# Kernel tuning notes

Hardware: AMD Instinct MI355X
Metric: run time of the kernel (lower is better)

## Reference

```python
import jax, jax.numpy as jnp
import numpy as np

HID = 1024
HEADS = 16
HEAD_DIM = HID // HEADS
MAX_REL = 2


def _rel_embed(table, length_q, length_k):
    # table: [2*MAX_REL+1, head_dim] -> [len_q, len_k, head_dim]
    dist = jnp.arange(length_k)[None, :] - jnp.arange(length_q)[:, None]
    idx = jnp.clip(dist, -MAX_REL, MAX_REL) + MAX_REL
    return table[idx]


def setup_inputs() -> dict:
    key = jax.random.key(0)
    ks = jax.random.split(key, 16)
    B, S = 2, 2048
    bound = 1.0 / np.sqrt(HID)

    def lin(k1, k2):
        W = jax.random.uniform(k1, (HID, HID), jnp.float32, -bound, bound)
        b = jax.random.uniform(k2, (HID,), jnp.float32, -bound, bound)
        return W, b

    Wq, bq = lin(ks[0], ks[1])
    Wk, bk = lin(ks[2], ks[3])
    Wv, bv = lin(ks[4], ks[5])
    Wo, bo = lin(ks[6], ks[7])
    # xavier_uniform for [5, head_dim] tables
    xav = np.sqrt(6.0 / (2 * MAX_REL + 1 + HEAD_DIM))
    rel_k = jax.random.uniform(ks[8], (2 * MAX_REL + 1, HEAD_DIM), jnp.float32, -xav, xav)
    rel_v = jax.random.uniform(ks[9], (2 * MAX_REL + 1, HEAD_DIM), jnp.float32, -xav, xav)
    return {
        'key': jax.random.normal(ks[10], (B, S, HID), jnp.float32),
        'query': jax.random.normal(ks[11], (B, S, HID), jnp.float32),
        'value': jax.random.normal(ks[12], (B, S, HID), jnp.float32),
        'Wq': Wq, 'bq': bq, 'Wk': Wk, 'bk': bk, 'Wv': Wv, 'bv': bv,
        'Wo': Wo, 'bo': bo, 'rel_k': rel_k, 'rel_v': rel_v,
    }


def reference(key, query, value, Wq, bq, Wk, bk, Wv, bv, Wo, bo, rel_k, rel_v):
    B, Lq, _ = query.shape
    Lk = key.shape[1]
    q = query @ Wq.T + bq   # [B, Lq, HID]
    k = key @ Wk.T + bk     # [B, Lk, HID]
    v = value @ Wv.T + bv   # [B, Lk, HID]

    qh = q.reshape(B, Lq, HEADS, HEAD_DIM).transpose(0, 2, 1, 3)  # [B,H,Lq,D]
    kh = k.reshape(B, Lk, HEADS, HEAD_DIM).transpose(0, 2, 1, 3)
    vh = v.reshape(B, Lk, HEADS, HEAD_DIM).transpose(0, 2, 1, 3)

    attn1 = jnp.einsum('bhqd,bhkd->bhqk', qh, kh)
    rk = _rel_embed(rel_k, Lq, Lk)                                # [Lq,Lk,D]
    attn2 = jnp.einsum('bhqd,qkd->bhqk', qh, rk)
    scale = jnp.sqrt(jnp.float32(HEAD_DIM))
    attn = jax.nn.softmax((attn1 + attn2) / scale, axis=-1)      # [B,H,Lq,Lk]

    w1 = jnp.einsum('bhqk,bhkd->bhqd', attn, vh)
    rv = _rel_embed(rel_v, Lq, Lk)                                # [Lq,Lk,D]
    w2 = jnp.einsum('bhqk,qkd->bhqd', attn, rv)

    x = (w1 + w2).transpose(0, 2, 1, 3).reshape(B, Lq, HID)
    return x @ Wo.T + bo
```

## Files before the change

kernel.cpp:

```cpp
#include <hip/hip_runtime.h>
#include <hip/hip_bf16.h>

#define S_LEN 2048
#define HID_DIM 1024
#define NH 16
#define HD 64
#define MTOT 4096

typedef __attribute__((ext_vector_type(8))) short short8;
typedef __attribute__((ext_vector_type(4))) float f32x4;

__device__ __forceinline__ float bf2f(unsigned short u) {
  union { unsigned int i; float f; } x; x.i = ((unsigned int)u) << 16; return x.f;
}
__device__ __forceinline__ unsigned short f2bf(float f) {
  union { float ff; unsigned int i; } x; x.ff = f;
  return (unsigned short)((x.i + 0x7fffu + ((x.i >> 16) & 1u)) >> 16);
}
__device__ __forceinline__ unsigned short f2bf_rna(float f) {
  union { float ff; unsigned int i; } x; x.ff = f;
  return (unsigned short)((x.i + 0x8000u) >> 16);
}
__device__ __forceinline__ f32x4 mfma16(short8 a, short8 b, f32x4 c) {
  return __builtin_amdgcn_mfma_f32_16x16x32_bf16(a, b, c, 0, 0, 0);
}
__device__ __forceinline__ void gl_lds16(const unsigned short* g, unsigned short* l) {
  __builtin_amdgcn_global_load_lds(
      (const __attribute__((address_space(1))) unsigned int*)g,
      (__attribute__((address_space(3))) unsigned int*)l, 16, 0, 0);
}

__global__ __launch_bounds__(256) void cvt3(const float* __restrict__ a, const float* __restrict__ b,
                                            const float* __restrict__ c, unsigned short* __restrict__ oa,
                                            unsigned short* __restrict__ ob, unsigned short* __restrict__ oc,
                                            int n4) {
  int i = blockIdx.x * 256 + threadIdx.x;
  if (i >= n4) return;
  const float* src = blockIdx.y == 0 ? a : blockIdx.y == 1 ? b : c;
  unsigned short* dst = blockIdx.y == 0 ? oa : blockIdx.y == 1 ? ob : oc;
  float4 v = reinterpret_cast<const float4*>(src)[i];
  union { unsigned short u[4]; unsigned long long ll; } o;
  o.u[0] = f2bf(v.x); o.u[1] = f2bf(v.y); o.u[2] = f2bf(v.z); o.u[3] = f2bf(v.w);
  reinterpret_cast<unsigned long long*>(dst)[i] = o.ll;
}
__global__ __launch_bounds__(256) void cvt4(const float* __restrict__ a, const float* __restrict__ b,
                                            const float* __restrict__ c, const float* __restrict__ d,
                                            unsigned short* __restrict__ oa, unsigned short* __restrict__ ob,
                                            unsigned short* __restrict__ oc, unsigned short* __restrict__ od,
                                            int n4) {
  int i = blockIdx.x * 256 + threadIdx.x;
  if (i >= n4) return;
  const float* src = blockIdx.y == 0 ? a : blockIdx.y == 1 ? b : blockIdx.y == 2 ? c : d;
  unsigned short* dst = blockIdx.y == 0 ? oa : blockIdx.y == 1 ? ob : blockIdx.y == 2 ? oc : od;
  float4 v = reinterpret_cast<const float4*>(src)[i];
  union { unsigned short u[4]; unsigned long long ll; } o;
  o.u[0] = f2bf(v.x); o.u[1] = f2bf(v.y); o.u[2] = f2bf(v.z); o.u[3] = f2bf(v.w);
  reinterpret_cast<unsigned long long*>(dst)[i] = o.ll;
}

__device__ __forceinline__ void gemm_core(const unsigned short* __restrict__ A,
                                          const unsigned short* __restrict__ W,
                                          unsigned short* As, unsigned short* Bs,
                                          int m0, int n0, f32x4 (&acc)[4][4]) {
  const int tid = threadIdx.x;
  const int lane = tid & 63;
  const int wrow = (tid >> 6) >> 1, wcol = (tid >> 6) & 1;
  const int lr = lane & 15, g = lane >> 4;
  const int r = tid >> 2, c8 = (tid & 3) * 8;
  const unsigned short* ag0 = A + (size_t)(m0 + r) * HID_DIM + c8;
  const unsigned short* ag1 = ag0 + (size_t)64 * HID_DIM;
  const unsigned short* bg0 = W + (size_t)(n0 + r) * HID_DIM + c8;
  const unsigned short* bg1 = bg0 + (size_t)64 * HID_DIM;
  unsigned short* al0 = As + r * 32 + c8;
  unsigned short* al1 = al0 + 64 * 32;
  unsigned short* bl0 = Bs + r * 32 + c8;
  unsigned short* bl1 = bl0 + 64 * 32;
  for (int k0 = 0; k0 < HID_DIM; k0 += 32) {
    __syncthreads();
    gl_lds16(ag0 + k0, al0);
    gl_lds16(ag1 + k0, al1);
    gl_lds16(bg0 + k0, bl0);
    gl_lds16(bg1 + k0, bl1);
    __syncthreads();
    short8 af[4], bfr[4];
#pragma unroll
    for (int m = 0; m < 4; ++m)
      af[m] = *reinterpret_cast<const short8*>(&As[(wrow * 64 + m * 16 + lr) * 32 + g * 8]);
#pragma unroll
    for (int n = 0; n < 4; ++n)
      bfr[n] = *reinterpret_cast<const short8*>(&Bs[(wcol * 64 + n * 16 + lr) * 32 + g * 8]);
#pragma unroll
    for (int m = 0; m < 4; ++m)
#pragma unroll
      for (int n = 0; n < 4; ++n)
        acc[m][n] = mfma16(af[m], bfr[n], acc[m][n]);
  }
}

__global__ __launch_bounds__(256) void qkv_gemm(
    const unsigned short* __restrict__ Aq, const unsigned short* __restrict__ Ak,
    const unsigned short* __restrict__ Av,
    const unsigned short* __restrict__ Wq, const unsigned short* __restrict__ Wk,
    const unsigned short* __restrict__ Wv,
    const float* __restrict__ bq, const float* __restrict__ bk, const float* __restrict__ bv,
    unsigned short* __restrict__ Qp, unsigned short* __restrict__ Kp,
    unsigned short* __restrict__ Vt) {
  __shared__ __attribute__((aligned(16))) unsigned short As[128 * 32];
  __shared__ __attribute__((aligned(16))) unsigned short Bs[128 * 32];
  const int which = blockIdx.x >> 3;
  const int n0 = (blockIdx.x & 7) * 128;
  const int m0 = blockIdx.y * 128;
  const unsigned short* A = which == 0 ? Aq : which == 1 ? Ak : Av;
  const unsigned short* W = which == 0 ? Wq : which == 1 ? Wk : Wv;
  const float* bias = which == 0 ? bq : which == 1 ? bk : bv;

  f32x4 acc[4][4];
  const f32x4 vzero = {0.f, 0.f, 0.f, 0.f};
#pragma unroll
  for (int m = 0; m < 4; ++m)
#pragma unroll
    for (int n = 0; n < 4; ++n) acc[m][n] = vzero;

  gemm_core(A, W, As, Bs, m0, n0, acc);

  const int lane = threadIdx.x & 63;
  const int wrow = (threadIdx.x >> 6) >> 1, wcol = (threadIdx.x >> 6) & 1;
  const int lr = lane & 15, g = lane >> 4;
  const float scl = (which == 0) ? 0.125f : 1.0f;
#pragma unroll
  for (int m = 0; m < 4; ++m) {
    const int rbase = m0 + wrow * 64 + m * 16 + g * 4;
#pragma unroll
    for (int n = 0; n < 4; ++n) {
      const int col = n0 + wcol * 64 + n * 16 + lr;
      const float bcol = bias[col];
      if (which < 2) {
        unsigned short* O = which == 0 ? Qp : Kp;
#pragma unroll
        for (int rg = 0; rg < 4; ++rg)
          O[(size_t)(rbase + rg) * HID_DIM + col] = f2bf((acc[m][n][rg] + bcol) * scl);
      } else {
        const int bb = rbase >> 11, s = rbase & 2047;
        const int h = col >> 6, d = col & 63;
        union { unsigned short u[4]; unsigned long long ll; } o;
#pragma unroll
        for (int rg = 0; rg < 4; ++rg) o.u[rg] = f2bf(acc[m][n][rg] + bcol);
        *reinterpret_cast<unsigned long long*>(
            &Vt[((size_t)(bb * NH + h) * HD + d) * S_LEN + s]) = o.ll;
      }
    }
  }
}

__global__ __launch_bounds__(256) void out_gemm(const unsigned short* __restrict__ X,
                                                const unsigned short* __restrict__ Wo,
                                                const float* __restrict__ bo,
                                                float* __restrict__ out) {
  __shared__ __attribute__((aligned(16))) unsigned short As[128 * 32];
  __shared__ __attribute__((aligned(16))) unsigned short Bs[128 * 32];
  const int n0 = blockIdx.x * 128;
  const int m0 = blockIdx.y * 128;
  f32x4 acc[4][4];
  const f32x4 vzero = {0.f, 0.f, 0.f, 0.f};
#pragma unroll
  for (int m = 0; m < 4; ++m)
#pragma unroll
    for (int n = 0; n < 4; ++n) acc[m][n] = vzero;

  gemm_core(X, Wo, As, Bs, m0, n0, acc);

  const int lane = threadIdx.x & 63;
  const int wrow = (threadIdx.x >> 6) >> 1, wcol = (threadIdx.x >> 6) & 1;
  const int lr = lane & 15, g = lane >> 4;
#pragma unroll
  for (int m = 0; m < 4; ++m) {
    const int rbase = m0 + wrow * 64 + m * 16 + g * 4;
#pragma unroll
    for (int n = 0; n < 4; ++n) {
      const int col = n0 + wcol * 64 + n * 16 + lr;
      const float bcol = bo[col];
#pragma unroll
      for (int rg = 0; rg < 4; ++rg)
        out[(size_t)(rbase + rg) * HID_DIM + col] = acc[m][n][rg] + bcol;
    }
  }
}

__global__ __launch_bounds__(512, 2) void attn_kernel(
    const unsigned short* __restrict__ Qp, const unsigned short* __restrict__ Kp,
    const unsigned short* __restrict__ Vt, const float* __restrict__ relk,
    const float* __restrict__ relv, unsigned short* __restrict__ Xa) {
  __shared__ __attribute__((aligned(16))) unsigned short kv[2][8192];
  __shared__ __attribute__((aligned(16))) unsigned short Ps[8][16][72];
  __shared__ float projs[128][5];
  __shared__ float relks[5][64];
  __shared__ float rvs[5][64];

  const int tid = threadIdx.x;
  const int lane = tid & 63;
  const int w = tid >> 6;
  const int lr = lane & 15, g = lane >> 4;
  const int virt = (blockIdx.x & 7) * 64 + (blockIdx.x >> 3);
  const int bh = virt >> 4;
  const int qbase = (virt & 15) * 128;
  const int b = bh >> 4, h = bh & 15;

  const unsigned short* Qg = Qp + ((size_t)(b * S_LEN + qbase)) * HID_DIM + h * HD;
  const unsigned short* Kg = Kp + ((size_t)b * S_LEN) * HID_DIM + h * HD;
  const unsigned short* Vg = Vt + (size_t)bh * HD * S_LEN;

#pragma unroll
  for (int i = 0; i < 2; ++i) {
    const int flat = i * 8192 + tid * 16;
    const int row = flat >> 7, c = (flat >> 4) & 7;
    gl_lds16(Qg + (size_t)row * HID_DIM + ((c ^ (row & 7)) * 8), &kv[1][flat >> 1]);
  }
  {
    const int flat = tid * 16;
    const int row = flat >> 7, c = (flat >> 4) & 7;
    const int csrc = (c ^ (row & 7)) * 8;
    gl_lds16(Kg + (size_t)row * HID_DIM + csrc, &kv[0][flat >> 1]);
    gl_lds16(Vg + (size_t)row * S_LEN + csrc, &kv[0][4096 + (flat >> 1)]);
  }
  for (int i = tid; i < 320; i += 512) {
    ((float*)relks)[i] = relk[i];
    ((float*)rvs)[i] = relv[i];
  }
  __syncthreads();

  for (int idx = tid; idx < 640; idx += 512) {
    const int row = idx & 127, j = idx >> 7;
    float acc = 0.f;
    for (int d = 0; d < 64; ++d)
      acc += bf2f(kv[1][row * 64 + ((d >> 3) ^ (row & 7)) * 8 + (d & 7)]) * relks[j][d];
    projs[row][j] = acc;
  }
  short8 aq[2];
#pragma unroll
  for (int h2 = 0; h2 < 2; ++h2) {
    const int row = w * 16 + lr;
    aq[h2] = *reinterpret_cast<const short8*>(
        &kv[1][row * 64 + (((g + 4 * h2) ^ (lr & 7)) * 8)]);
  }
  __syncthreads();

  float pj0[4], pj4[4];
#pragma unroll
  for (int i = 0; i < 4; ++i) {
    const int qloc = w * 16 + g * 4 + i;
    pj0[i] = projs[qloc][0];
    pj4[i] = projs[qloc][4];
  }

  const f32x4 vzero = {0.f, 0.f, 0.f, 0.f};
  f32x4 accO[4];
#pragma unroll
  for (int n = 0; n < 4; ++n) accO[n] = vzero;
  float sp0[4], sp4[4], sv1[4], sv2[4], sv3[4];
#pragma unroll
  for (int i = 0; i < 4; ++i) {
    sp0[i] = 0.f; sp4[i] = 0.f; sv1[i] = 0.f; sv2[i] = 0.f; sv3[i] = 0.f;
  }
  const int Qw = qbase + w * 16;

  for (int t = 0; t < 32; ++t) {
    const int kb = t * 64;
    const unsigned short* Ks = kv[t & 1];
    const unsigned short* Vs = Ks + 4096;
    if (t < 31) {
      const int kb2 = kb + 64;
      unsigned short* dst = &kv[(t + 1) & 1][0];
      const int flat = tid * 16;
      const int row = flat >> 7, c = (flat >> 4) & 7;
      const int csrc = (c ^ (row & 7)) * 8;
      gl_lds16(Kg + (size_t)(kb2 + row) * HID_DIM + csrc, dst + (flat >> 1));
      gl_lds16(Vg + (size_t)row * S_LEN + kb2 + csrc, dst + 4096 + (flat >> 1));
    }
    short8 kf[4][2];
#pragma unroll
    for (int n = 0; n < 4; ++n)
#pragma unroll
      for (int h2 = 0; h2 < 2; ++h2)
        kf[n][h2] = *reinterpret_cast<const short8*>(
            &Ks[(n * 16 + lr) * 64 + (((g + 4 * h2) ^ (lr & 7)) * 8)]);
    f32x4 accS[4];
#pragma unroll
    for (int n = 0; n < 4; ++n) {
      f32x4 z = mfma16(aq[0], kf[n][0], vzero);
      accS[n] = mfma16(aq[1], kf[n][1], z);
    }

    const bool mixed = (kb + 63 >= Qw - 2) && (kb <= Qw + 17);
    if (!mixed) {
      const bool left = kb < Qw;
#pragma unroll
      for (int n = 0; n < 4; ++n)
#pragma unroll
        for (int r = 0; r < 4; ++r) {
          const float p = __expf(accS[n][r] + (left ? pj0[r] : pj4[r]));
          if (left) sp0[r] += p; else sp4[r] += p;
          Ps[w][g * 4 + r][n * 16 + lr] = f2bf_rna(p);
        }
    } else {
#pragma unroll
      for (int n = 0; n < 4; ++n) {
        const int kg = kb + n * 16 + lr;
#pragma unroll
        for (int r = 0; r < 4; ++r) {
          const int qloc = w * 16 + g * 4 + r;
          const int dist = kg - (qbase + qloc);
          float pjv;
          if (dist <= -2) pjv = pj0[r];
          else if (dist >= 2) pjv = pj4[r];
          else pjv = projs[qloc][dist + 2];
          const float p = __expf(accS[n][r] + pjv);
          if (dist <= -2) sp0[r] += p;
          else if (dist >= 2) sp4[r] += p;
          else if (dist == -1) sv1[r] += p;
          else if (dist == 0) sv2[r] += p;
          else sv3[r] += p;
          Ps[w][g * 4 + r][n * 16 + lr] = f2bf_rna(p);
        }
      }
    }
    asm volatile("" ::: "memory");
    short8 vf[4][2];
#pragma unroll
    for (int n = 0; n < 4; ++n)
#pragma unroll
      for (int h2 = 0; h2 < 2; ++h2)
        vf[n][h2] = *reinterpret_cast<const short8*>(
            &Vs[(n * 16 + lr) * 64 + (((g + 4 * h2) ^ (lr & 7)) * 8)]);
    short8 pa0 = *reinterpret_cast<const short8*>(&Ps[w][lr][g * 8]);
    short8 pa1 = *reinterpret_cast<const short8*>(&Ps[w][lr][g * 8 + 32]);
#pragma unroll
    for (int n = 0; n < 4; ++n) {
      accO[n] = mfma16(pa0, vf[n][0], accO[n]);
      accO[n] = mfma16(pa1, vf[n][1], accO[n]);
    }
    __syncthreads();
  }

#pragma unroll
  for (int i = 0; i < 4; ++i) {
    float v0 = sp0[i], v1 = sv1[i], v2 = sv2[i], v3 = sv3[i], v4 = sp4[i];
#pragma unroll
    for (int s = 1; s <= 8; s <<= 1) {
      v0 += __shfl_xor(v0, s); v1 += __shfl_xor(v1, s); v2 += __shfl_xor(v2, s);
      v3 += __shfl_xor(v3, s); v4 += __shfl_xor(v4, s);
    }
    const float rl = 1.f / (v0 + v1 + v2 + v3 + v4);
    const int qrow = b * S_LEN + qbase + w * 16 + g * 4 + i;
#pragma unroll
    for (int n = 0; n < 4; ++n) {
      const int d = n * 16 + lr;
      const float val = (accO[n][i] + v0 * rvs[0][d] + v1 * rvs[1][d] +
                         v2 * rvs[2][d] + v3 * rvs[3][d] + v4 * rvs[4][d]) * rl;
      Xa[(size_t)qrow * HID_DIM + h * HD + d] = f2bf(val);
    }
  }
}

extern "C" void kernel_launch(void* const* d_in, const int* in_sizes, int n_in,
                              void* d_out, int out_size, void* d_ws, size_t ws_size,
                              hipStream_t stream) {
  (void)in_sizes; (void)n_in; (void)out_size; (void)ws_size;
  const float* f_key   = (const float*)d_in[0];
  const float* f_query = (const float*)d_in[1];
  const float* f_value = (const float*)d_in[2];
  const float* Wq = (const float*)d_in[3];
  const float* bq = (const float*)d_in[4];
  const float* Wk = (const float*)d_in[5];
  const float* bk = (const float*)d_in[6];
  const float* Wv = (const float*)d_in[7];
  const float* bv = (const float*)d_in[8];
  const float* Wo = (const float*)d_in[9];
  const float* bo = (const float*)d_in[10];
  const float* relk = (const float*)d_in[11];
  const float* relv = (const float*)d_in[12];

  char* ws = (char*)d_ws;
  const size_t SZ = (size_t)MTOT * HID_DIM * sizeof(unsigned short);
  unsigned short* cq  = (unsigned short*)(ws + 0 * SZ);
  unsigned short* ck  = (unsigned short*)(ws + 1 * SZ);
  unsigned short* cv  = (unsigned short*)(ws + 2 * SZ);
  unsigned short* wqb = (unsigned short*)(ws + 3 * SZ);
  unsigned short* wkb = wqb + 1024 * 1024;
  unsigned short* wvb = wkb + 1024 * 1024;
  unsigned short* wob = wvb + 1024 * 1024;
  unsigned short* Qp  = (unsigned short*)(ws + 4 * SZ);
  unsigned short* Kp  = (unsigned short*)(ws + 5 * SZ);
  unsigned short* Vt  = (unsigned short*)(ws + 6 * SZ);
  unsigned short* xa  = cq;

  const int nIn4 = MTOT * HID_DIM / 4;
  const int nW4 = 1024 * 1024 / 4;
  cvt3<<<dim3(nIn4 / 256, 3), 256, 0, stream>>>(f_query, f_key, f_value, cq, ck, cv, nIn4);
  cvt4<<<dim3(nW4 / 256, 4), 256, 0, stream>>>(Wq, Wk, Wv, Wo, wqb, wkb, wvb, wob, nW4);
  qkv_gemm<<<dim3(24, 32), dim3(256), 0, stream>>>(cq, ck, cv, wqb, wkb, wvb, bq, bk, bv,
                                                   Qp, Kp, Vt);
  attn_kernel<<<dim3(512), dim3(512), 0, stream>>>(Qp, Kp, Vt, relk, relv, xa);
  out_gemm<<<dim3(8, 32), dim3(256), 0, stream>>>(xa, wob, bo, (float*)d_out);
}
```

Measured before the change: 169.7 us.

## Widen GEMM K-tile to 64 with XOR-swizzled LDS and fold rel-bias into MFMA

The shared GEMM core for the QKV and output projections now stages a 64-wide K slice per iteration instead of 32. It uses an XOR-swizzled LDS layout to avoid bank conflicts, which halves the number of barrier pairs and doubles LDS usage per block. The attention kernel also seeds the score MFMA accumulator with the per-row relative-position bias for non-diagonal tiles. This removes a separate add per score element before the exponential.

```diff
diff --git a/kernel.cpp b/kernel.cpp
--- a/kernel.cpp
+++ b/kernel.cpp
@@ -66,34 +66,37 @@
   const int lane = tid & 63;
   const int wrow = (tid >> 6) >> 1, wcol = (tid >> 6) & 1;
   const int lr = lane & 15, g = lane >> 4;
-  const int r = tid >> 2, c8 = (tid & 3) * 8;
-  const unsigned short* ag0 = A + (size_t)(m0 + r) * HID_DIM + c8;
-  const unsigned short* ag1 = ag0 + (size_t)64 * HID_DIM;
-  const unsigned short* bg0 = W + (size_t)(n0 + r) * HID_DIM + c8;
-  const unsigned short* bg1 = bg0 + (size_t)64 * HID_DIM;
-  unsigned short* al0 = As + r * 32 + c8;
-  unsigned short* al1 = al0 + 64 * 32;
-  unsigned short* bl0 = Bs + r * 32 + c8;
-  unsigned short* bl1 = bl0 + 64 * 32;
-  for (int k0 = 0; k0 < HID_DIM; k0 += 32) {
+  const int r32 = tid >> 3;
+  const int cph = (tid & 7) ^ (r32 & 7);
+  const unsigned short* ag = A + (size_t)(m0 + r32) * HID_DIM + cph * 8;
+  const unsigned short* bg = W + (size_t)(n0 + r32) * HID_DIM + cph * 8;
+  unsigned short* al = As + tid * 8;
+  unsigned short* bl = Bs + tid * 8;
+  for (int k0 = 0; k0 < HID_DIM; k0 += 64) {
     __syncthreads();
-    gl_lds16(ag0 + k0, al0);
-    gl_lds16(ag1 + k0, al1);
-    gl_lds16(bg0 + k0, bl0);
-    gl_lds16(bg1 + k0, bl1);
+#pragma unroll
+    for (int p = 0; p < 4; ++p) {
+      gl_lds16(ag + (size_t)(p * 32) * HID_DIM + k0, al + p * 2048);
+      gl_lds16(bg + (size_t)(p * 32) * HID_DIM + k0, bl + p * 2048);
+    }
     __syncthreads();
-    short8 af[4], bfr[4];
-#pragma unroll
-    for (int m = 0; m < 4; ++m)
-      af[m] = *reinterpret_cast<const short8*>(&As[(wrow * 64 + m * 16 + lr) * 32 + g * 8]);
-#pragma unroll
-    for (int n = 0; n < 4; ++n)
-      bfr[n] = *reinterpret_cast<const short8*>(&Bs[(wcol * 64 + n * 16 + lr) * 32 + g * 8]);
-#pragma unroll
-    for (int m = 0; m < 4; ++m)
+#pragma unroll
+    for (int ks = 0; ks < 2; ++ks) {
+      short8 af[4], bfr[4];
+#pragma unroll
+      for (int m = 0; m < 4; ++m)
+        af[m] = *reinterpret_cast<const short8*>(
+            &As[(wrow * 64 + m * 16 + lr) * 64 + (((ks * 4 + g) ^ (lr & 7)) * 8)]);
 #pragma unroll
       for (int n = 0; n < 4; ++n)
-        acc[m][n] = mfma16(af[m], bfr[n], acc[m][n]);
+        bfr[n] = *reinterpret_cast<const short8*>(
+            &Bs[(wcol * 64 + n * 16 + lr) * 64 + (((ks * 4 + g) ^ (lr & 7)) * 8)]);
+#pragma unroll
+      for (int m = 0; m < 4; ++m)
+#pragma unroll
+        for (int n = 0; n < 4; ++n)
+          acc[m][n] = mfma16(af[m], bfr[n], acc[m][n]);
+    }
   }
 }
 
@@ -105,8 +108,8 @@
     const float* __restrict__ bq, const float* __restrict__ bk, const float* __restrict__ bv,
     unsigned short* __restrict__ Qp, unsigned short* __restrict__ Kp,
     unsigned short* __restrict__ Vt) {
-  __shared__ __attribute__((aligned(16))) unsigned short As[128 * 32];
-  __shared__ __attribute__((aligned(16))) unsigned short Bs[128 * 32];
+  __shared__ __attribute__((aligned(16))) unsigned short As[128 * 64];
+  __shared__ __attribute__((aligned(16))) unsigned short Bs[128 * 64];
   const int which = blockIdx.x >> 3;
   const int n0 = (blockIdx.x & 7) * 128;
   const int m0 = blockIdx.y * 128;
@@ -156,8 +159,8 @@
                                                 const unsigned short* __restrict__ Wo,
                                                 const float* __restrict__ bo,
                                                 float* __restrict__ out) {
-  __shared__ __attribute__((aligned(16))) unsigned short As[128 * 32];
-  __shared__ __attribute__((aligned(16))) unsigned short Bs[128 * 32];
+  __shared__ __attribute__((aligned(16))) unsigned short As[128 * 64];
+  __shared__ __attribute__((aligned(16))) unsigned short Bs[128 * 64];
   const int n0 = blockIdx.x * 128;
   const int m0 = blockIdx.y * 128;
   f32x4 acc[4][4];
@@ -251,6 +254,9 @@
     pj0[i] = projs[qloc][0];
     pj4[i] = projs[qloc][4];
   }
+  f32x4 cinitL, cinitR;
+#pragma unroll
+  for (int i = 0; i < 4; ++i) { cinitL[i] = pj0[i]; cinitR[i] = pj4[i]; }
 
   const f32x4 vzero = {0.f, 0.f, 0.f, 0.f};
   f32x4 accO[4];
@@ -276,6 +282,9 @@
       gl_lds16(Kg + (size_t)(kb2 + row) * HID_DIM + csrc, dst + (flat >> 1));
       gl_lds16(Vg + (size_t)row * S_LEN + kb2 + csrc, dst + 4096 + (flat >> 1));
     }
+    const bool mixed = (kb + 63 >= Qw - 2) && (kb <= Qw + 17);
+    const bool left = kb < Qw;
+    const f32x4 ci = mixed ? vzero : (left ? cinitL : cinitR);
     short8 kf[4][2];
 #pragma unroll
     for (int n = 0; n < 4; ++n)
@@ -286,18 +295,16 @@
     f32x4 accS[4];
 #pragma unroll
     for (int n = 0; n < 4; ++n) {
-      f32x4 z = mfma16(aq[0], kf[n][0], vzero);
+      f32x4 z = mfma16(aq[0], kf[n][0], ci);
       accS[n] = mfma16(aq[1], kf[n][1], z);
     }
 
-    const bool mixed = (kb + 63 >= Qw - 2) && (kb <= Qw + 17);
     if (!mixed) {
-      const bool left = kb < Qw;
 #pragma unroll
       for (int n = 0; n < 4; ++n)
 #pragma unroll
         for (int r = 0; r < 4; ++r) {
-          const float p = __expf(accS[n][r] + (left ? pj0[r] : pj4[r]));
+          const float p = __expf(accS[n][r]);
           if (left) sp0[r] += p; else sp4[r] += p;
           Ps[w][g * 4 + r][n * 16 + lr] = f2bf_rna(p);
         }
```

New measurement: 153.5 us. 9.6% less time.
